# Performance work log

Measured on AMD Instinct MI355X. Metric: run time of the kernel, lower is better.

## Reference

```python
import jax, jax.numpy as jnp
import numpy as np

N, T, F = 20000, 8, 128
E = 320000
H_GCN, H_CONV, H_LSTM = 32, 64, 128


def setup_inputs() -> dict:
    key = jax.random.key(0)
    ks = jax.random.split(key, 16)
    s = lambda k, shape: jax.random.normal(k, shape, dtype=jnp.float32) * 0.05
    inp = {
        'x': jax.random.normal(ks[0], (N, T, F), dtype=jnp.float32),
        'edge_index': jax.random.randint(ks[1], (2, E), 0, N, dtype=jnp.int32),
        'gcn_W': s(ks[2], (F, H_GCN)),
        'gcn_b': s(ks[3], (H_GCN,)),
        'conv_W': s(ks[4], (H_CONV, H_GCN, 2)),
        'conv_b': s(ks[5], (H_CONV,)),
        'W_ih': s(ks[6], (4 * H_LSTM, H_CONV)),
        'W_hh': s(ks[7], (4 * H_LSTM, H_LSTM)),
        'b_ih': s(ks[8], (4 * H_LSTM,)),
        'b_hh': s(ks[9], (4 * H_LSTM,)),
        'fc1_W': s(ks[10], (64, H_LSTM)),
        'fc1_b': s(ks[11], (64,)),
        'fc2_W': s(ks[12], (F, 64)),
        'fc2_b': s(ks[13], (F,)),
    }
    return inp


def _forward(x, edge_index, gcn_W, gcn_b, conv_W, conv_b, W_ih, W_hh, b_ih, b_hh, fc1_W, fc1_b, fc2_W, fc2_b):
    n = x.shape[0]
    # ---- GCNConv (PyG semantics: linear, add self-loops, sym-normalized aggregate) ----
    loops = jnp.arange(n, dtype=edge_index.dtype)
    row = jnp.concatenate([edge_index[0], loops])  # source
    col = jnp.concatenate([edge_index[1], loops])  # target
    deg = jax.ops.segment_sum(jnp.ones_like(col, dtype=x.dtype), col, num_segments=n)
    dinv = jax.lax.rsqrt(deg)  # deg >= 1 thanks to self-loops
    norm = dinv[row] * dinv[col]  # [E+N]
    h = jnp.einsum('ntf,fo->nto', x, gcn_W)  # transform once for all timesteps
    msg = h[row] * norm[:, None, None]  # [E+N, T, 32]
    agg = jax.ops.segment_sum(msg, col, num_segments=n) + gcn_b
    g = jax.nn.relu(agg)  # [N, T, 32]; dropout is identity at inference
    # ---- Conv1d(32->64, k=2) over time ----
    xc = jnp.transpose(g, (0, 2, 1))  # [N, 32, T]
    y = jax.lax.conv_general_dilated(xc, conv_W, window_strides=(1,), padding='VALID',
                                     dimension_numbers=('NCH', 'OIH', 'NCH'))
    y = jax.nn.relu(y + conv_b[None, :, None])  # [N, 64, T-1]
    seq = jnp.transpose(y, (2, 0, 1))  # [T-1, N, 64]
    # ---- LSTM (torch gate order i, f, g, o) ----
    def step(carry, xt):
        hp, cp = carry
        z = xt @ W_ih.T + hp @ W_hh.T + (b_ih + b_hh)  # [N, 4H]
        i, f, gg, o = jnp.split(z, 4, axis=-1)
        c = jax.nn.sigmoid(f) * cp + jax.nn.sigmoid(i) * jnp.tanh(gg)
        hn = jax.nn.sigmoid(o) * jnp.tanh(c)
        return (hn, c), None
    h0 = jnp.zeros((n, H_LSTM), dtype=x.dtype)
    (hT, _), _ = jax.lax.scan(step, (h0, h0), seq)
    # ---- Head ----
    out = jax.nn.relu(hT @ fc1_W.T + fc1_b)
    out = jax.nn.sigmoid(out @ fc2_W.T + fc2_b)
    return out  # [N, num_features]


def reference(x, edge_index, gcn_W, gcn_b, conv_W, conv_b, W_ih, W_hh, b_ih, b_hh, fc1_W, fc1_b, fc2_W, fc2_b):
    return _forward(x, edge_index, gcn_W, gcn_b, conv_W, conv_b, W_ih, W_hh, b_ih, b_hh, fc1_W, fc1_b, fc2_W, fc2_b)
```

## Files before the change

### kernel.cpp

```cpp
#include <hip/hip_runtime.h>
#include <hip/hip_bf16.h>

#define T_STEPS 8
#define F_IN    128
#define H_GCN   32
#define H_CONV  64
#define H_LSTM  128

typedef __bf16 bf16x8 __attribute__((ext_vector_type(8)));
typedef float  f32x4  __attribute__((ext_vector_type(4)));
typedef unsigned short ushort8v __attribute__((ext_vector_type(8)));

#if __has_builtin(__builtin_amdgcn_exp2f)
__device__ __forceinline__ float exp2_f(float x) { return __builtin_amdgcn_exp2f(x); }
#else
__device__ __forceinline__ float exp2_f(float x) { return exp2f(x); }
#endif
#if __has_builtin(__builtin_amdgcn_rcpf)
__device__ __forceinline__ float rcp_f(float x) { return __builtin_amdgcn_rcpf(x); }
#else
__device__ __forceinline__ float rcp_f(float x) { return 1.f / x; }
#endif

#define NL2E  (-1.442695041f)
#define NL2E2 (-2.885390082f)

__device__ __forceinline__ float sigm_fast(float x) {
  return rcp_f(1.f + exp2_f(x * NL2E));
}

__device__ __forceinline__ float ubf(unsigned short u) {
  union { unsigned int i; float f; } v; v.i = ((unsigned int)u) << 16; return v.f;
}
__device__ __forceinline__ unsigned short bfb(float f) {
  __hip_bfloat16 b = __float2bfloat16(f);
  return __builtin_bit_cast(unsigned short, b);
}

__device__ __forceinline__ bf16x8 load_bf8(const __hip_bfloat16* p) {
  int4 v = *reinterpret_cast<const int4*>(p);
  return __builtin_bit_cast(bf16x8, v);
}

__global__ __launch_bounds__(256) void k_transform(const float* __restrict__ x,
                                                   const __hip_bfloat16* __restrict__ Wgt,
                                                   const float* __restrict__ dinv,
                                                   __hip_bfloat16* __restrict__ hs)
{
  int tid  = threadIdx.x;
  int wave = tid >> 6;
  int lane = tid & 63;
  int l15  = lane & 15;
  int lhi  = lane >> 4;
  long r0  = (long)blockIdx.x * 64 + wave * 16;

  bf16x8 bw[2][4];
  #pragma unroll
  for (int ct = 0; ct < 2; ++ct)
    #pragma unroll
    for (int ks = 0; ks < 4; ++ks)
      bw[ct][ks] = load_bf8(Wgt + (ct * 16 + l15) * 128 + ks * 32 + lhi * 8);

  const float* xp = x + (r0 + l15) * 128 + lhi * 8;
  f32x4 acc[2];
  acc[0] = (f32x4){0.f, 0.f, 0.f, 0.f};
  acc[1] = (f32x4){0.f, 0.f, 0.f, 0.f};

  #pragma unroll
  for (int ks = 0; ks < 4; ++ks) {
    float4 v0 = *reinterpret_cast<const float4*>(xp + ks * 32);
    float4 v1 = *reinterpret_cast<const float4*>(xp + ks * 32 + 4);
    bf16x8 a;
    a[0] = (__bf16)v0.x; a[1] = (__bf16)v0.y; a[2] = (__bf16)v0.z; a[3] = (__bf16)v0.w;
    a[4] = (__bf16)v1.x; a[5] = (__bf16)v1.y; a[6] = (__bf16)v1.z; a[7] = (__bf16)v1.w;
    acc[0] = __builtin_amdgcn_mfma_f32_16x16x32_bf16(a, bw[0][ks], acc[0], 0, 0, 0);
    acc[1] = __builtin_amdgcn_mfma_f32_16x16x32_bf16(a, bw[1][ks], acc[1], 0, 0, 0);
  }

  #pragma unroll
  for (int r = 0; r < 4; ++r) {
    long rr = r0 + lhi * 4 + r;
    float dv = dinv[rr >> 3];
    hs[rr * 32 + l15]      = __float2bfloat16(acc[0][r] * dv);
    hs[rr * 32 + 16 + l15] = __float2bfloat16(acc[1][r] * dv);
  }
}

__global__ void k_count_init(const int* __restrict__ col, int* __restrict__ cnt, int E,
                             int* __restrict__ adj, int N, int padE,
                             unsigned int* __restrict__ hz)
{
  int i = blockIdx.x * 256 + threadIdx.x;
  if (i < E) atomicAdd(&cnt[col[i]], 1);
  if (i < padE) adj[i] = N;
  int j = i - padE;
  if (j >= 0 && j < 128) hz[j] = 0u;
}

__global__ __launch_bounds__(1024) void k_scan(const int* __restrict__ cnt,
                                               int* __restrict__ row_ptr,
                                               int* __restrict__ cursor,
                                               float* __restrict__ dinv, int N)
{
  __shared__ int s[1024];
  int tid = threadIdx.x;
  const int CH = (N + 1023) >> 10;
  int i0 = tid * CH;
  int sum = 0;
  for (int j = 0; j < CH; ++j) {
    int i = i0 + j;
    if (i < N) sum += (cnt[i] + 15) & ~15;
  }
  s[tid] = sum;
  __syncthreads();
  #pragma unroll
  for (int off = 1; off < 1024; off <<= 1) {
    int t = (tid >= off) ? s[tid - off] : 0;
    __syncthreads();
    s[tid] += t;
    __syncthreads();
  }
  int run = (tid > 0) ? s[tid - 1] : 0;
  for (int j = 0; j < CH; ++j) {
    int i = i0 + j;
    if (i < N) {
      int v = cnt[i];
      cursor[i] = run;
      row_ptr[i] = run;
      dinv[i] = rsqrtf((float)v + 1.0f);
      run += (v + 15) & ~15;
      if (i == N - 1) row_ptr[N] = run;
    }
  }
}

__global__ void k_fill(const int* __restrict__ ei, int* __restrict__ cursor,
                       int* __restrict__ adj, int E)
{
  int e = blockIdx.x * 256 + threadIdx.x;
  if (e < E) {
    int r = ei[e], c = ei[E + e];
    int pos = atomicAdd(&cursor[c], 1);
    adj[pos] = r;
  }
}

__global__ __launch_bounds__(256) void k_gather(
    const int* __restrict__ row_ptr, const int* __restrict__ adj,
    const float* __restrict__ dinv, const __hip_bfloat16* __restrict__ hs,
    const float* __restrict__ gcnb,
    __hip_bfloat16* __restrict__ g, int N)
{
  int tid  = threadIdx.x;
  int wave = tid >> 6;
  int lane = tid & 63;

  int n = blockIdx.x * 4 + wave;
  int start = row_ptr[n], end = row_ptr[n + 1];
  float dn = dinv[n];

  const __hip_bfloat16* hl = hs + lane * 4;
  float acc0, acc1, acc2, acc3;
  {
    ushort4 hv = *reinterpret_cast<const ushort4*>(hl + (size_t)n * 256);
    acc0 = ubf(hv.x); acc1 = ubf(hv.y); acc2 = ubf(hv.z); acc3 = ubf(hv.w);
  }

  for (int base = start; base < end; base += 16) {
    int s0 = adj[base + 0],  s1 = adj[base + 1],  s2 = adj[base + 2],  s3 = adj[base + 3];
    int s4 = adj[base + 4],  s5 = adj[base + 5],  s6 = adj[base + 6],  s7 = adj[base + 7];
    int s8 = adj[base + 8],  s9 = adj[base + 9],  sa = adj[base + 10], sb = adj[base + 11];
    int sc = adj[base + 12], sd = adj[base + 13], se = adj[base + 14], sf = adj[base + 15];
    ushort4 r0 = *reinterpret_cast<const ushort4*>(hl + (size_t)s0 * 256);
    ushort4 r1 = *reinterpret_cast<const ushort4*>(hl + (size_t)s1 * 256);
    ushort4 r2 = *reinterpret_cast<const ushort4*>(hl + (size_t)s2 * 256);
    ushort4 r3 = *reinterpret_cast<const ushort4*>(hl + (size_t)s3 * 256);
    ushort4 r4 = *reinterpret_cast<const ushort4*>(hl + (size_t)s4 * 256);
    ushort4 r5 = *reinterpret_cast<const ushort4*>(hl + (size_t)s5 * 256);
    ushort4 r6 = *reinterpret_cast<const ushort4*>(hl + (size_t)s6 * 256);
    ushort4 r7 = *reinterpret_cast<const ushort4*>(hl + (size_t)s7 * 256);
    ushort4 r8 = *reinterpret_cast<const ushort4*>(hl + (size_t)s8 * 256);
    ushort4 r9 = *reinterpret_cast<const ushort4*>(hl + (size_t)s9 * 256);
    ushort4 ra = *reinterpret_cast<const ushort4*>(hl + (size_t)sa * 256);
    ushort4 rb = *reinterpret_cast<const ushort4*>(hl + (size_t)sb * 256);
    ushort4 rc = *reinterpret_cast<const ushort4*>(hl + (size_t)sc * 256);
    ushort4 rd = *reinterpret_cast<const ushort4*>(hl + (size_t)sd * 256);
    ushort4 re = *reinterpret_cast<const ushort4*>(hl + (size_t)se * 256);
    ushort4 rf = *reinterpret_cast<const ushort4*>(hl + (size_t)sf * 256);
    acc0 += ((ubf(r0.x) + ubf(r1.x)) + (ubf(r2.x) + ubf(r3.x))) + ((ubf(r4.x) + ubf(r5.x)) + (ubf(r6.x) + ubf(r7.x)))
          + ((ubf(r8.x) + ubf(r9.x)) + (ubf(ra.x) + ubf(rb.x))) + ((ubf(rc.x) + ubf(rd.x)) + (ubf(re.x) + ubf(rf.x)));
    acc1 += ((ubf(r0.y) + ubf(r1.y)) + (ubf(r2.y) + ubf(r3.y))) + ((ubf(r4.y) + ubf(r5.y)) + (ubf(r6.y) + ubf(r7.y)))
          + ((ubf(r8.y) + ubf(r9.y)) + (ubf(ra.y) + ubf(rb.y))) + ((ubf(rc.y) + ubf(rd.y)) + (ubf(re.y) + ubf(rf.y)));
    acc2 += ((ubf(r0.z) + ubf(r1.z)) + (ubf(r2.z) + ubf(r3.z))) + ((ubf(r4.z) + ubf(r5.z)) + (ubf(r6.z) + ubf(r7.z)))
          + ((ubf(r8.z) + ubf(r9.z)) + (ubf(ra.z) + ubf(rb.z))) + ((ubf(rc.z) + ubf(rd.z)) + (ubf(re.z) + ubf(rf.z)));
    acc3 += ((ubf(r0.w) + ubf(r1.w)) + (ubf(r2.w) + ubf(r3.w))) + ((ubf(r4.w) + ubf(r5.w)) + (ubf(r6.w) + ubf(r7.w)))
          + ((ubf(r8.w) + ubf(r9.w)) + (ubf(ra.w) + ubf(rb.w))) + ((ubf(rc.w) + ubf(rd.w)) + (ubf(re.w) + ubf(rf.w)));
  }

  int ci0 = (lane * 4) & 31;
  ushort4 o;
  o.x = bfb(fmaxf(fmaf(acc0, dn, gcnb[ci0 + 0]), 0.f));
  o.y = bfb(fmaxf(fmaf(acc1, dn, gcnb[ci0 + 1]), 0.f));
  o.z = bfb(fmaxf(fmaf(acc2, dn, gcnb[ci0 + 2]), 0.f));
  o.w = bfb(fmaxf(fmaf(acc3, dn, gcnb[ci0 + 3]), 0.f));
  *reinterpret_cast<ushort4*>(g + (size_t)n * 256 + lane * 4) = o;
}

__global__ __launch_bounds__(256) void k_conv(
    const __hip_bfloat16* __restrict__ g,
    const __hip_bfloat16* __restrict__ Wcb,
    const float* __restrict__ bc,
    __hip_bfloat16* __restrict__ seq, int N)
{
  __shared__ __hip_bfloat16 A[4][16][72];
  int tid  = threadIdx.x;
  int wave = tid >> 6;
  int lane = tid & 63;
  int l15  = lane & 15;
  int lhi  = lane >> 4;

  if (tid < 144) {
    int w = tid / 36, q = tid % 36;
    int row = 14 + q / 18, cc = (q % 18) * 4;
    *reinterpret_cast<uint2*>(&A[w][row][cc]) = make_uint2(0u, 0u);
  }

  {
    int f0 = tid * 8;
    ushort8v v = *reinterpret_cast<const ushort8v*>(g + (size_t)blockIdx.x * 2048 + f0);
    int n_local = f0 >> 8;
    int rem     = f0 & 255;
    int t_row   = rem >> 5;
    int ci0     = rem & 31;
    int w       = n_local >> 1;
    int rbase   = (n_local & 1) * 7;
    #pragma unroll
    for (int e = 0; e < 8; ++e) {
      unsigned short u = v[e];
      int k0 = (ci0 + e) * 2;
      if (t_row <= 6)
        *reinterpret_cast<unsigned short*>(&A[w][rbase + t_row][k0]) = u;
      if (t_row >= 1)
        *reinterpret_cast<unsigned short*>(&A[w][rbase + t_row - 1][k0 + 1]) = u;
    }
  }
  __syncthreads();

  bf16x8 bfr[2][4];
  #pragma unroll
  for (int ks = 0; ks < 2; ++ks)
    #pragma unroll
    for (int cg = 0; cg < 4; ++cg)
      bfr[ks][cg] = load_bf8(Wcb + (cg * 16 + l15) * 64 + ks * 32 + lhi * 8);

  f32x4 acc[4];
  #pragma unroll
  for (int cg = 0; cg < 4; ++cg) acc[cg] = (f32x4){0.f, 0.f, 0.f, 0.f};

  #pragma unroll
  for (int ks = 0; ks < 2; ++ks) {
    bf16x8 a = load_bf8(&A[wave][l15][ks * 32 + lhi * 8]);
    #pragma unroll
    for (int cg = 0; cg < 4; ++cg)
      acc[cg] = __builtin_amdgcn_mfma_f32_16x16x32_bf16(a, bfr[ks][cg], acc[cg], 0, 0, 0);
  }

  long n64 = (long)N * 64;
  #pragma unroll
  for (int r = 0; r < 4; ++r) {
    int rr = lhi * 4 + r;
    if (rr < 14) {
      int hi = rr >= 7 ? 1 : 0;
      int nl = wave * 2 + hi;
      int t  = rr - 7 * hi;
      long n = (long)blockIdx.x * 8 + nl;
      #pragma unroll
      for (int cg = 0; cg < 4; ++cg) {
        int co = cg * 16 + l15;
        seq[(long)t * n64 + n * 64 + co] = __float2bfloat16(fmaxf(acc[cg][r] + bc[co], 0.f));
      }
    }
  }
}

__global__ __launch_bounds__(256) void k_prep(const float* __restrict__ Wih, const float* __restrict__ Whh,
                       const float* __restrict__ bih, const float* __restrict__ bhh,
                       const float* __restrict__ fc1W, const float* __restrict__ fc2W,
                       const float* __restrict__ convW, const float* __restrict__ gcnW,
                       __hip_bfloat16* __restrict__ Wcat, float* __restrict__ bias,
                       __hip_bfloat16* __restrict__ W1b, __hip_bfloat16* __restrict__ W2b,
                       __hip_bfloat16* __restrict__ Wcb, __hip_bfloat16* __restrict__ Wgt)
{
  int i = blockIdx.x * 256 + threadIdx.x;
  if (i < 512 * 192) {
    int q = i / 192, k = i - q * 192;
    float v = (k < 64) ? Wih[q * 64 + k] : Whh[q * 128 + (k - 64)];
    Wcat[i] = __float2bfloat16(v);
  } else if (i < 512 * 192 + 64 * 128) {
    int j = i - 512 * 192;
    W1b[j] = __float2bfloat16(fc1W[j]);
  } else if (i < 512 * 192 + 64 * 128 + 128 * 64) {
    int j = i - 512 * 192 - 64 * 128;
    W2b[j] = __float2bfloat16(fc2W[j]);
  } else if (i < 512 * 192 + 64 * 128 + 128 * 64 + 64 * 64) {
    int j = i - 512 * 192 - 64 * 128 - 128 * 64;
    Wcb[j] = __float2bfloat16(convW[j]);
  } else if (i < 512 * 192 + 64 * 128 + 128 * 64 + 64 * 64 + 32 * 128) {
    int j = i - 512 * 192 - 64 * 128 - 128 * 64 - 64 * 64;
    int o = j >> 7, f = j & 127;
    Wgt[j] = __float2bfloat16(gcnW[f * 32 + o]);
  } else if (i < 512 * 192 + 64 * 128 + 128 * 64 + 64 * 64 + 32 * 128 + 512) {
    int j = i - 512 * 192 - 64 * 128 - 128 * 64 - 64 * 64 - 32 * 128;
    bias[j] = bih[j] + bhh[j];
  }
}

__global__ __launch_bounds__(512, 2) void k_lstm_head(
    const __hip_bfloat16* __restrict__ seq,
    const __hip_bfloat16* __restrict__ Wcat,
    const float* __restrict__ bias,
    const __hip_bfloat16* __restrict__ W1b,
    const float* __restrict__ fc1b,
    const __hip_bfloat16* __restrict__ W2b,
    const float* __restrict__ fc2b,
    float* __restrict__ out, int N)
{
  __shared__ __hip_bfloat16 h_lds[2][16][136];
  __shared__ __hip_bfloat16 s1_lds[16][72];
  int tid  = threadIdx.x;
  int wave = tid >> 6;
  int lane = tid & 63;
  int l15  = lane & 15;
  int lhi  = lane >> 4;
  long n0  = (long)blockIdx.x * 16;
  int hc   = wave * 16 + l15;

  bf16x8 bw[6][4];
  #pragma unroll
  for (int ks = 0; ks < 6; ++ks)
    #pragma unroll
    for (int gg = 0; gg < 4; ++gg)
      bw[ks][gg] = load_bf8(Wcat + (size_t)(gg * 128 + hc) * 192 + ks * 32 + lhi * 8);

  float kbi = bias[hc]       * NL2E;
  float kbf = bias[128 + hc] * NL2E;
  float kbg = bias[256 + hc] * NL2E2;
  float kbo = bias[384 + hc] * NL2E;
  float c[4] = {0.f, 0.f, 0.f, 0.f};

  const __hip_bfloat16* sp = seq + (n0 + l15) * 64 + lhi * 8;
  size_t tstr = (size_t)N * 64;
  bf16x8 ax0 = load_bf8(sp);
  bf16x8 ax1 = load_bf8(sp + 32);

  for (int t = 0; t < 7; ++t) {
    bf16x8 nx0, nx1;
    if (t < 6) {
      nx0 = load_bf8(sp + (size_t)(t + 1) * tstr);
      nx1 = load_bf8(sp + (size_t)(t + 1) * tstr + 32);
    }
    f32x4 acc[4];
    #pragma unroll
    for (int gg = 0; gg < 4; ++gg) acc[gg] = (f32x4){0.f, 0.f, 0.f, 0.f};

    #pragma unroll
    for (int gg = 0; gg < 4; ++gg)
      acc[gg] = __builtin_amdgcn_mfma_f32_16x16x32_bf16(ax0, bw[0][gg], acc[gg], 0, 0, 0);
    #pragma unroll
    for (int gg = 0; gg < 4; ++gg)
      acc[gg] = __builtin_amdgcn_mfma_f32_16x16x32_bf16(ax1, bw[1][gg], acc[gg], 0, 0, 0);

    if (t > 0) {
      const __hip_bfloat16* hb = &h_lds[(t + 1) & 1][0][0];
      #pragma unroll
      for (int ks = 2; ks < 6; ++ks) {
        bf16x8 a = load_bf8(hb + l15 * 136 + (ks - 2) * 32 + lhi * 8);
        #pragma unroll
        for (int gg = 0; gg < 4; ++gg)
          acc[gg] = __builtin_amdgcn_mfma_f32_16x16x32_bf16(a, bw[ks][gg], acc[gg], 0, 0, 0);
      }
    }

    __hip_bfloat16* hw = &h_lds[t & 1][0][0];
    #pragma unroll
    for (int r = 0; r < 4; ++r) {
      float si  = rcp_f(1.f + exp2_f(fmaf(acc[0][r], NL2E,  kbi)));
      float sf  = rcp_f(1.f + exp2_f(fmaf(acc[1][r], NL2E,  kbf)));
      float sg2 = rcp_f(1.f + exp2_f(fmaf(acc[2][r], NL2E2, kbg)));
      float so  = rcp_f(1.f + exp2_f(fmaf(acc[3][r], NL2E,  kbo)));
      float tg  = fmaf(2.f, sg2, -1.f);
      float cn  = fmaf(sf, c[r], si * tg);
      c[r] = cn;
      float sc2 = rcp_f(1.f + exp2_f(cn * NL2E2));
      float hn  = so * fmaf(2.f, sc2, -1.f);
      hw[(lhi * 4 + r) * 136 + hc] = __float2bfloat16(hn);
    }
    __syncthreads();

    ax0 = nx0; ax1 = nx1;
  }

  if (wave < 4) {
    int col1 = wave * 16 + l15;
    f32x4 acc1 = (f32x4){0.f, 0.f, 0.f, 0.f};
    #pragma unroll
    for (int ks = 0; ks < 4; ++ks) {
      int kb = ks * 32 + lhi * 8;
      bf16x8 a = load_bf8(&h_lds[0][l15][kb]);
      bf16x8 b = load_bf8(W1b + col1 * 128 + kb);
      acc1 = __builtin_amdgcn_mfma_f32_16x16x32_bf16(a, b, acc1, 0, 0, 0);
    }
    float b1 = fc1b[col1];
    #pragma unroll
    for (int r = 0; r < 4; ++r)
      s1_lds[lhi * 4 + r][col1] = __float2bfloat16(fmaxf(acc1[r] + b1, 0.f));
  }
  __syncthreads();

  {
    int c2 = wave * 16 + l15;
    f32x4 acc2 = (f32x4){0.f, 0.f, 0.f, 0.f};
    #pragma unroll
    for (int ks = 0; ks < 2; ++ks) {
      int kb = ks * 32 + lhi * 8;
      bf16x8 a = load_bf8(&s1_lds[l15][kb]);
      bf16x8 b = load_bf8(W2b + c2 * 64 + kb);
      acc2 = __builtin_amdgcn_mfma_f32_16x16x32_bf16(a, b, acc2, 0, 0, 0);
    }
    float b2 = fc2b[c2];
    #pragma unroll
    for (int r = 0; r < 4; ++r)
      out[(n0 + lhi * 4 + r) * 128 + c2] = sigm_fast(acc2[r] + b2);
  }
}

extern "C" void kernel_launch(void* const* d_in, const int* in_sizes, int n_in,
                              void* d_out, int out_size, void* d_ws, size_t ws_size,
                              hipStream_t stream)
{
  const float* x     = (const float*)d_in[0];
  const int*   ei    = (const int*)d_in[1];
  const float* gcnW  = (const float*)d_in[2];
  const float* gcnb  = (const float*)d_in[3];
  const float* convW = (const float*)d_in[4];
  const float* convb = (const float*)d_in[5];
  const float* Wih   = (const float*)d_in[6];
  const float* Whh   = (const float*)d_in[7];
  const float* bih   = (const float*)d_in[8];
  const float* bhh   = (const float*)d_in[9];
  const float* fc1W  = (const float*)d_in[10];
  const float* fc1b  = (const float*)d_in[11];
  const float* fc2W  = (const float*)d_in[12];
  const float* fc2b  = (const float*)d_in[13];

  const int N = in_sizes[0] / (T_STEPS * F_IN);
  const int E = in_sizes[1] / 2;
  const int padE = E + 16 * N;

  char* ws = (char*)d_ws;
  size_t off = 0;
  auto alloc = [&](size_t bytes) {
    void* p = ws + off;
    off = (off + bytes + 255) & ~(size_t)255;
    return p;
  };
  __hip_bfloat16* hs  = (__hip_bfloat16*)alloc((size_t)(N + 1) * 256 * 2);
  __hip_bfloat16* g   = (__hip_bfloat16*)alloc((size_t)N * 256 * 2);
  __hip_bfloat16* seq = (__hip_bfloat16*)alloc((size_t)7 * N * 64 * 2);
  int* cnt     = (int*)alloc((size_t)N * 4);
  int* row_ptr = (int*)alloc((size_t)(N + 1) * 4);
  int* cursor  = (int*)alloc((size_t)N * 4);
  float* dinv  = (float*)alloc((size_t)N * 4);
  int* adj     = (int*)alloc((size_t)padE * 4);
  __hip_bfloat16* Wcat = (__hip_bfloat16*)alloc(512 * 192 * 2);
  float* bias = (float*)alloc(512 * 4);
  __hip_bfloat16* W1b = (__hip_bfloat16*)alloc(64 * 128 * 2);
  __hip_bfloat16* W2b = (__hip_bfloat16*)alloc(128 * 64 * 2);
  __hip_bfloat16* Wcb = (__hip_bfloat16*)alloc(64 * 64 * 2);
  __hip_bfloat16* Wgt = (__hip_bfloat16*)alloc(32 * 128 * 2);

  hipMemsetAsync(cnt, 0, (size_t)N * 4, stream);

  const int PREP_TOT = 512 * 192 + 64 * 128 + 128 * 64 + 64 * 64 + 32 * 128 + 512;
  k_prep<<<(PREP_TOT + 255) / 256, 256, 0, stream>>>(Wih, Whh, bih, bhh, fc1W, fc2W, convW, gcnW,
                                                     Wcat, bias, W1b, W2b, Wcb, Wgt);
  k_count_init<<<(padE + 128 + 255) / 256, 256, 0, stream>>>(
      ei + E, cnt, E, adj, N, padE, (unsigned int*)(hs + (size_t)N * 256));
  k_scan<<<1, 1024, 0, stream>>>(cnt, row_ptr, cursor, dinv, N);
  k_transform<<<(N * T_STEPS) / 64, 256, 0, stream>>>(x, Wgt, dinv, hs);
  k_fill<<<(E + 255) / 256, 256, 0, stream>>>(ei, cursor, adj, E);
  k_gather<<<N / 4, 256, 0, stream>>>(row_ptr, adj, dinv, hs, gcnb, g, N);
  k_conv<<<N / 8, 256, 0, stream>>>(g, Wcb, convb, seq, N);
  k_lstm_head<<<N / 16, 512, 0, stream>>>(seq, Wcat, bias, W1b, fc1b, W2b, fc2b, (float*)d_out, N);
}
```

Before: 221.8 us.

## Process 32 nodes per LSTM block to reuse register-resident weights

The LSTM+head kernel now handles two 16-row node tiles per block instead of one, sharing the register-held W_ih/W_hh fragments across both tiles and halving the block count. This amortizes each block's load of the weight fragments and gives the MFMA units two independent accumulator chains to interleave. The head is reshaped so all 8 waves participate. In exchange, register pressure rises (double accumulators and cell state) under launch_bounds(512,2), which risks spills or lower occupancy. N/32 blocks also assumes N divides by 32.

Measured after the change: 216.4 us. -2.4%, faster.

```diff
diff --git a/kernel.cpp b/kernel.cpp
--- a/kernel.cpp
+++ b/kernel.cpp
@@ -325,14 +325,14 @@
     const float* __restrict__ fc2b,
     float* __restrict__ out, int N)
 {
-  __shared__ __hip_bfloat16 h_lds[2][16][136];
-  __shared__ __hip_bfloat16 s1_lds[16][72];
+  __shared__ __hip_bfloat16 h_lds[2][32][136];
+  __shared__ __hip_bfloat16 s1_lds[32][72];
   int tid  = threadIdx.x;
   int wave = tid >> 6;
   int lane = tid & 63;
   int l15  = lane & 15;
   int lhi  = lane >> 4;
-  long n0  = (long)blockIdx.x * 16;
+  long n0  = (long)blockIdx.x * 32;
   int hc   = wave * 16 + l15;
 
   bf16x8 bw[6][4];
@@ -346,91 +346,121 @@
   float kbf = bias[128 + hc] * NL2E;
   float kbg = bias[256 + hc] * NL2E2;
   float kbo = bias[384 + hc] * NL2E;
-  float c[4] = {0.f, 0.f, 0.f, 0.f};
-
-  const __hip_bfloat16* sp = seq + (n0 + l15) * 64 + lhi * 8;
+  float c0[4] = {0.f, 0.f, 0.f, 0.f};
+  float c1[4] = {0.f, 0.f, 0.f, 0.f};
+
+  const __hip_bfloat16* sp0 = seq + (n0 +      l15) * 64 + lhi * 8;
+  const __hip_bfloat16* sp1 = seq + (n0 + 16 + l15) * 64 + lhi * 8;
   size_t tstr = (size_t)N * 64;
-  bf16x8 ax0 = load_bf8(sp);
-  bf16x8 ax1 = load_bf8(sp + 32);
+  bf16x8 ax00 = load_bf8(sp0), ax01 = load_bf8(sp0 + 32);
+  bf16x8 ax10 = load_bf8(sp1), ax11 = load_bf8(sp1 + 32);
 
   for (int t = 0; t < 7; ++t) {
-    bf16x8 nx0, nx1;
+    bf16x8 nx00, nx01, nx10, nx11;
     if (t < 6) {
-      nx0 = load_bf8(sp + (size_t)(t + 1) * tstr);
-      nx1 = load_bf8(sp + (size_t)(t + 1) * tstr + 32);
-    }
-    f32x4 acc[4];
-    #pragma unroll
-    for (int gg = 0; gg < 4; ++gg) acc[gg] = (f32x4){0.f, 0.f, 0.f, 0.f};
-
-    #pragma unroll
-    for (int gg = 0; gg < 4; ++gg)
-      acc[gg] = __builtin_amdgcn_mfma_f32_16x16x32_bf16(ax0, bw[0][gg], acc[gg], 0, 0, 0);
-    #pragma unroll
-    for (int gg = 0; gg < 4; ++gg)
-      acc[gg] = __builtin_amdgcn_mfma_f32_16x16x32_bf16(ax1, bw[1][gg], acc[gg], 0, 0, 0);
+      nx00 = load_bf8(sp0 + (size_t)(t + 1) * tstr);
+      nx01 = load_bf8(sp0 + (size_t)(t + 1) * tstr + 32);
+      nx10 = load_bf8(sp1 + (size_t)(t + 1) * tstr);
+      nx11 = load_bf8(sp1 + (size_t)(t + 1) * tstr + 32);
+    }
+    f32x4 acc0[4], acc1[4];
+    #pragma unroll
+    for (int gg = 0; gg < 4; ++gg) {
+      acc0[gg] = (f32x4){0.f, 0.f, 0.f, 0.f};
+      acc1[gg] = (f32x4){0.f, 0.f, 0.f, 0.f};
+    }
+
+    #pragma unroll
+    for (int gg = 0; gg < 4; ++gg) {
+      acc0[gg] = __builtin_amdgcn_mfma_f32_16x16x32_bf16(ax00, bw[0][gg], acc0[gg], 0, 0, 0);
+      acc1[gg] = __builtin_amdgcn_mfma_f32_16x16x32_bf16(ax10, bw[0][gg], acc1[gg], 0, 0, 0);
+    }
+    #pragma unroll
+    for (int gg = 0; gg < 4; ++gg) {
+      acc0[gg] = __builtin_amdgcn_mfma_f32_16x16x32_bf16(ax01, bw[1][gg], acc0[gg], 0, 0, 0);
+      acc1[gg] = __builtin_amdgcn_mfma_f32_16x16x32_bf16(ax11, bw[1][gg], acc1[gg], 0, 0, 0);
+    }
 
     if (t > 0) {
       const __hip_bfloat16* hb = &h_lds[(t + 1) & 1][0][0];
       #pragma unroll
       for (int ks = 2; ks < 6; ++ks) {
-        bf16x8 a = load_bf8(hb + l15 * 136 + (ks - 2) * 32 + lhi * 8);
+        bf16x8 a0 = load_bf8(hb + (     l15) * 136 + (ks - 2) * 32 + lhi * 8);
+        bf16x8 a1 = load_bf8(hb + (16 + l15) * 136 + (ks - 2) * 32 + lhi * 8);
         #pragma unroll
-        for (int gg = 0; gg < 4; ++gg)
-          acc[gg] = __builtin_amdgcn_mfma_f32_16x16x32_bf16(a, bw[ks][gg], acc[gg], 0, 0, 0);
+        for (int gg = 0; gg < 4; ++gg) {
+          acc0[gg] = __builtin_amdgcn_mfma_f32_16x16x32_bf16(a0, bw[ks][gg], acc0[gg], 0, 0, 0);
+          acc1[gg] = __builtin_amdgcn_mfma_f32_16x16x32_bf16(a1, bw[ks][gg], acc1[gg], 0, 0, 0);
+        }
       }
     }
 
     __hip_bfloat16* hw = &h_lds[t & 1][0][0];
     #pragma unroll
     for (int r = 0; r < 4; ++r) {
-      float si  = rcp_f(1.f + exp2_f(fmaf(acc[0][r], NL2E,  kbi)));
-      float sf  = rcp_f(1.f + exp2_f(fmaf(acc[1][r], NL2E,  kbf)));
-      float sg2 = rcp_f(1.f + exp2_f(fmaf(acc[2][r], NL2E2, kbg)));
-      float so  = rcp_f(1.f + exp2_f(fmaf(acc[3][r], NL2E,  kbo)));
+      float si  = rcp_f(1.f + exp2_f(fmaf(acc0[0][r], NL2E,  kbi)));
+      float sf  = rcp_f(1.f + exp2_f(fmaf(acc0[1][r], NL2E,  kbf)));
+      float sg2 = rcp_f(1.f + exp2_f(fmaf(acc0[2][r], NL2E2, kbg)));
+      float so  = rcp_f(1.f + exp2_f(fmaf(acc0[3][r], NL2E,  kbo)));
       float tg  = fmaf(2.f, sg2, -1.f);
-      float cn  = fmaf(sf, c[r], si * tg);
-      c[r] = cn;
+      float cn  = fmaf(sf, c0[r], si * tg);
+      c0[r] = cn;
       float sc2 = rcp_f(1.f + exp2_f(cn * NL2E2));
-      float hn  = so * fmaf(2.f, sc2, -1.f);
-      hw[(lhi * 4 + r) * 136 + hc] = __float2bfloat16(hn);
+      hw[(lhi * 4 + r) * 136 + hc] = __float2bfloat16(so * fmaf(2.f, sc2, -1.f));
+    }
+    #pragma unroll
+    for (int r = 0; r < 4; ++r) {
+      float si  = rcp_f(1.f + exp2_f(fmaf(acc1[0][r], NL2E,  kbi)));
+      float sf  = rcp_f(1.f + exp2_f(fmaf(acc1[1][r], NL2E,  kbf)));
+      float sg2 = rcp_f(1.f + exp2_f(fmaf(acc1[2][r], NL2E2, kbg)));
+      float so  = rcp_f(1.f + exp2_f(fmaf(acc1[3][r], NL2E,  kbo)));
+      float tg  = fmaf(2.f, sg2, -1.f);
+      float cn  = fmaf(sf, c1[r], si * tg);
+      c1[r] = cn;
+      float sc2 = rcp_f(1.f + exp2_f(cn * NL2E2));
+      hw[(16 + lhi * 4 + r) * 136 + hc] = __float2bfloat16(so * fmaf(2.f, sc2, -1.f));
     }
     __syncthreads();
 
-    ax0 = nx0; ax1 = nx1;
-  }
-
-  if (wave < 4) {
-    int col1 = wave * 16 + l15;
-    f32x4 acc1 = (f32x4){0.f, 0.f, 0.f, 0.f};
+    ax00 = nx00; ax01 = nx01; ax10 = nx10; ax11 = nx11;
+  }
+
+  {
+    int m1   = wave >> 2;
+    int col1 = (wave & 3) * 16 + l15;
+    f32x4 acc1v = (f32x4){0.f, 0.f, 0.f, 0.f};
     #pragma unroll
     for (int ks = 0; ks < 4; ++ks) {
       int kb = ks * 32 + lhi * 8;
-      bf16x8 a = load_bf8(&h_lds[0][l15][kb]);
+      bf16x8 a = load_bf8(&h_lds[0][m1 * 16 + l15][kb]);
       bf16x8 b = load_bf8(W1b + col1 * 128 + kb);
-      acc1 = __builtin_amdgcn_mfma_f32_16x16x32_bf16(a, b, acc1, 0, 0, 0);
+      acc1v = __builtin_amdgcn_mfma_f32_16x16x32_bf16(a, b, acc1v, 0, 0, 0);
     }
     float b1 = fc1b[col1];
     #pragma unroll
     for (int r = 0; r < 4; ++r)
-      s1_lds[lhi * 4 + r][col1] = __float2bfloat16(fmaxf(acc1[r] + b1, 0.f));
+      s1_lds[m1 * 16 + lhi * 4 + r][col1] = __float2bfloat16(fmaxf(acc1v[r] + b1, 0.f));
   }
   __syncthreads();
 
   {
-    int c2 = wave * 16 + l15;
-    f32x4 acc2 = (f32x4){0.f, 0.f, 0.f, 0.f};
-    #pragma unroll
-    for (int ks = 0; ks < 2; ++ks) {
-      int kb = ks * 32 + lhi * 8;
-      bf16x8 a = load_bf8(&s1_lds[l15][kb]);
-      bf16x8 b = load_bf8(W2b + c2 * 64 + kb);
-      acc2 = __builtin_amdgcn_mfma_f32_16x16x32_bf16(a, b, acc2, 0, 0, 0);
-    }
-    float b2 = fc2b[c2];
-    #pragma unroll
-    for (int r = 0; r < 4; ++r)
-      out[(n0 + lhi * 4 + r) * 128 + c2] = sigm_fast(acc2[r] + b2);
+    int m2 = wave >> 2;
+    #pragma unroll
+    for (int half = 0; half < 2; ++half) {
+      int c2 = (wave & 3) * 16 + half * 64 + l15;
+      f32x4 acc2 = (f32x4){0.f, 0.f, 0.f, 0.f};
+      #pragma unroll
+      for (int ks = 0; ks < 2; ++ks) {
+        int kb = ks * 32 + lhi * 8;
+        bf16x8 a = load_bf8(&s1_lds[m2 * 16 + l15][kb]);
+        bf16x8 b = load_bf8(W2b + c2 * 64 + kb);
+        acc2 = __builtin_amdgcn_mfma_f32_16x16x32_bf16(a, b, acc2, 0, 0, 0);
+      }
+      float b2 = fc2b[c2];
+      #pragma unroll
+      for (int r = 0; r < 4; ++r)
+        out[(n0 + m2 * 16 + lhi * 4 + r) * 128 + c2] = sigm_fast(acc2[r] + b2);
+    }
   }
 }
 
@@ -491,5 +521,5 @@
   k_fill<<<(E + 255) / 256, 256, 0, stream>>>(ei, cursor, adj, E);
   k_gather<<<N / 4, 256, 0, stream>>>(row_ptr, adj, dinv, hs, gcnb, g, N);
   k_conv<<<N / 8, 256, 0, stream>>>(g, Wcb, convb, seq, N);
-  k_lstm_head<<<N / 16, 512, 0, stream>>>(seq, Wcat, bias, W1b, fc1b, W2b, fc2b, (float*)d_out, N);
-}
+  k_lstm_head<<<N / 32, 512, 0, stream>>>(seq, Wcat, bias, W1b, fc1b, W2b, fc2b, (float*)d_out, N);
+}
```

## Process 80 nodes per LSTM block to amortize register-resident weights

Applied to the files above, without the earlier changes.

The LSTM+head kernel now handles five 16-node tiles per block instead of one, reusing the register-held Wcat fragments across all five tiles and cutting the grid from N/16 to N/80 blocks (250 blocks). This amortizes the per-block weight loads and gives each wave more independent MFMA work per barrier. In exchange, accumulator and cell-state register usage grows by about 5x, which may cause spills under launch_bounds(512,2). The small grid may also leave many of the GPU's CUs idle. The next-timestep input prefetch was dropped as well.

Result: faster. 205.2 us (-7.5%).

```diff
diff --git a/kernel.cpp b/kernel.cpp
--- a/kernel.cpp
+++ b/kernel.cpp
@@ -325,14 +325,14 @@
     const float* __restrict__ fc2b,
     float* __restrict__ out, int N)
 {
-  __shared__ __hip_bfloat16 h_lds[2][16][136];
-  __shared__ __hip_bfloat16 s1_lds[16][72];
+  __shared__ __hip_bfloat16 h_lds[2][80][136];
+  __shared__ __hip_bfloat16 s1_lds[80][72];
   int tid  = threadIdx.x;
   int wave = tid >> 6;
   int lane = tid & 63;
   int l15  = lane & 15;
   int lhi  = lane >> 4;
-  long n0  = (long)blockIdx.x * 16;
+  long n0  = (long)blockIdx.x * 80;
   int hc   = wave * 16 + l15;
 
   bf16x8 bw[6][4];
@@ -346,91 +346,106 @@
   float kbf = bias[128 + hc] * NL2E;
   float kbg = bias[256 + hc] * NL2E2;
   float kbo = bias[384 + hc] * NL2E;
-  float c[4] = {0.f, 0.f, 0.f, 0.f};
-
-  const __hip_bfloat16* sp = seq + (n0 + l15) * 64 + lhi * 8;
+  float c[5][4];
+  #pragma unroll
+  for (int g = 0; g < 5; ++g)
+    #pragma unroll
+    for (int r = 0; r < 4; ++r) c[g][r] = 0.f;
+
   size_t tstr = (size_t)N * 64;
-  bf16x8 ax0 = load_bf8(sp);
-  bf16x8 ax1 = load_bf8(sp + 32);
+  const __hip_bfloat16* spb = seq + (n0 + l15) * 64 + lhi * 8;
 
   for (int t = 0; t < 7; ++t) {
-    bf16x8 nx0, nx1;
-    if (t < 6) {
-      nx0 = load_bf8(sp + (size_t)(t + 1) * tstr);
-      nx1 = load_bf8(sp + (size_t)(t + 1) * tstr + 32);
-    }
-    f32x4 acc[4];
-    #pragma unroll
-    for (int gg = 0; gg < 4; ++gg) acc[gg] = (f32x4){0.f, 0.f, 0.f, 0.f};
-
-    #pragma unroll
-    for (int gg = 0; gg < 4; ++gg)
-      acc[gg] = __builtin_amdgcn_mfma_f32_16x16x32_bf16(ax0, bw[0][gg], acc[gg], 0, 0, 0);
-    #pragma unroll
-    for (int gg = 0; gg < 4; ++gg)
-      acc[gg] = __builtin_amdgcn_mfma_f32_16x16x32_bf16(ax1, bw[1][gg], acc[gg], 0, 0, 0);
+    f32x4 acc[5][4];
+    #pragma unroll
+    for (int g = 0; g < 5; ++g)
+      #pragma unroll
+      for (int gg = 0; gg < 4; ++gg)
+        acc[g][gg] = (f32x4){0.f, 0.f, 0.f, 0.f};
+
+    #pragma unroll
+    for (int g = 0; g < 5; ++g) {
+      const __hip_bfloat16* sp = spb + (size_t)t * tstr + (size_t)g * 16 * 64;
+      bf16x8 a0 = load_bf8(sp);
+      bf16x8 a1 = load_bf8(sp + 32);
+      #pragma unroll
+      for (int gg = 0; gg < 4; ++gg)
+        acc[g][gg] = __builtin_amdgcn_mfma_f32_16x16x32_bf16(a0, bw[0][gg], acc[g][gg], 0, 0, 0);
+      #pragma unroll
+      for (int gg = 0; gg < 4; ++gg)
+        acc[g][gg] = __builtin_amdgcn_mfma_f32_16x16x32_bf16(a1, bw[1][gg], acc[g][gg], 0, 0, 0);
+    }
 
     if (t > 0) {
       const __hip_bfloat16* hb = &h_lds[(t + 1) & 1][0][0];
       #pragma unroll
       for (int ks = 2; ks < 6; ++ks) {
-        bf16x8 a = load_bf8(hb + l15 * 136 + (ks - 2) * 32 + lhi * 8);
         #pragma unroll
-        for (int gg = 0; gg < 4; ++gg)
-          acc[gg] = __builtin_amdgcn_mfma_f32_16x16x32_bf16(a, bw[ks][gg], acc[gg], 0, 0, 0);
+        for (int g = 0; g < 5; ++g) {
+          bf16x8 a = load_bf8(hb + (g * 16 + l15) * 136 + (ks - 2) * 32 + lhi * 8);
+          #pragma unroll
+          for (int gg = 0; gg < 4; ++gg)
+            acc[g][gg] = __builtin_amdgcn_mfma_f32_16x16x32_bf16(a, bw[ks][gg], acc[g][gg], 0, 0, 0);
+        }
       }
     }
 
     __hip_bfloat16* hw = &h_lds[t & 1][0][0];
     #pragma unroll
-    for (int r = 0; r < 4; ++r) {
-      float si  = rcp_f(1.f + exp2_f(fmaf(acc[0][r], NL2E,  kbi)));
-      float sf  = rcp_f(1.f + exp2_f(fmaf(acc[1][r], NL2E,  kbf)));
-      float sg2 = rcp_f(1.f + exp2_f(fmaf(acc[2][r], NL2E2, kbg)));
-      float so  = rcp_f(1.f + exp2_f(fmaf(acc[3][r], NL2E,  kbo)));
-      float tg  = fmaf(2.f, sg2, -1.f);
-      float cn  = fmaf(sf, c[r], si * tg);
-      c[r] = cn;
-      float sc2 = rcp_f(1.f + exp2_f(cn * NL2E2));
-      float hn  = so * fmaf(2.f, sc2, -1.f);
-      hw[(lhi * 4 + r) * 136 + hc] = __float2bfloat16(hn);
+    for (int g = 0; g < 5; ++g) {
+      #pragma unroll
+      for (int r = 0; r < 4; ++r) {
+        float si  = rcp_f(1.f + exp2_f(fmaf(acc[g][0][r], NL2E,  kbi)));
+        float sf  = rcp_f(1.f + exp2_f(fmaf(acc[g][1][r], NL2E,  kbf)));
+        float sg2 = rcp_f(1.f + exp2_f(fmaf(acc[g][2][r], NL2E2, kbg)));
+        float so  = rcp_f(1.f + exp2_f(fmaf(acc[g][3][r], NL2E,  kbo)));
+        float tg  = fmaf(2.f, sg2, -1.f);
+        float cn  = fmaf(sf, c[g][r], si * tg);
+        c[g][r] = cn;
+        float sc2 = rcp_f(1.f + exp2_f(cn * NL2E2));
+        hw[(g * 16 + lhi * 4 + r) * 136 + hc] = __float2bfloat16(so * fmaf(2.f, sc2, -1.f));
+      }
     }
     __syncthreads();
-
-    ax0 = nx0; ax1 = nx1;
   }
 
   if (wave < 4) {
     int col1 = wave * 16 + l15;
-    f32x4 acc1 = (f32x4){0.f, 0.f, 0.f, 0.f};
-    #pragma unroll
-    for (int ks = 0; ks < 4; ++ks) {
-      int kb = ks * 32 + lhi * 8;
-      bf16x8 a = load_bf8(&h_lds[0][l15][kb]);
-      bf16x8 b = load_bf8(W1b + col1 * 128 + kb);
-      acc1 = __builtin_amdgcn_mfma_f32_16x16x32_bf16(a, b, acc1, 0, 0, 0);
-    }
     float b1 = fc1b[col1];
     #pragma unroll
-    for (int r = 0; r < 4; ++r)
-      s1_lds[lhi * 4 + r][col1] = __float2bfloat16(fmaxf(acc1[r] + b1, 0.f));
+    for (int g = 0; g < 5; ++g) {
+      f32x4 acc1v = (f32x4){0.f, 0.f, 0.f, 0.f};
+      #pragma unroll
+      for (int ks = 0; ks < 4; ++ks) {
+        int kb = ks * 32 + lhi * 8;
+        bf16x8 a = load_bf8(&h_lds[0][g * 16 + l15][kb]);
+        bf16x8 b = load_bf8(W1b + col1 * 128 + kb);
+        acc1v = __builtin_amdgcn_mfma_f32_16x16x32_bf16(a, b, acc1v, 0, 0, 0);
+      }
+      #pragma unroll
+      for (int r = 0; r < 4; ++r)
+        s1_lds[g * 16 + lhi * 4 + r][col1] = __float2bfloat16(fmaxf(acc1v[r] + b1, 0.f));
+    }
   }
   __syncthreads();
 
   {
     int c2 = wave * 16 + l15;
-    f32x4 acc2 = (f32x4){0.f, 0.f, 0.f, 0.f};
-    #pragma unroll
-    for (int ks = 0; ks < 2; ++ks) {
-      int kb = ks * 32 + lhi * 8;
-      bf16x8 a = load_bf8(&s1_lds[l15][kb]);
-      bf16x8 b = load_bf8(W2b + c2 * 64 + kb);
-      acc2 = __builtin_amdgcn_mfma_f32_16x16x32_bf16(a, b, acc2, 0, 0, 0);
-    }
     float b2 = fc2b[c2];
     #pragma unroll
-    for (int r = 0; r < 4; ++r)
-      out[(n0 + lhi * 4 + r) * 128 + c2] = sigm_fast(acc2[r] + b2);
+    for (int g = 0; g < 5; ++g) {
+      f32x4 acc2 = (f32x4){0.f, 0.f, 0.f, 0.f};
+      #pragma unroll
+      for (int ks = 0; ks < 2; ++ks) {
+        int kb = ks * 32 + lhi * 8;
+        bf16x8 a = load_bf8(&s1_lds[g * 16 + l15][kb]);
+        bf16x8 b = load_bf8(W2b + c2 * 64 + kb);
+        acc2 = __builtin_amdgcn_mfma_f32_16x16x32_bf16(a, b, acc2, 0, 0, 0);
+      }
+      #pragma unroll
+      for (int r = 0; r < 4; ++r)
+        out[(n0 + g * 16 + lhi * 4 + r) * 128 + c2] = sigm_fast(acc2[r] + b2);
+    }
   }
 }
 
@@ -491,5 +506,5 @@
   k_fill<<<(E + 255) / 256, 256, 0, stream>>>(ei, cursor, adj, E);
   k_gather<<<N / 4, 256, 0, stream>>>(row_ptr, adj, dinv, hs, gcnb, g, N);
   k_conv<<<N / 8, 256, 0, stream>>>(g, Wcb, convb, seq, N);
-  k_lstm_head<<<N / 16, 512, 0, stream>>>(seq, Wcat, bias, W1b, fc1b, W2b, fc2b, (float*)d_out, N);
-}
+  k_lstm_head<<<N / 80, 512, 0, stream>>>(seq, Wcat, bias, W1b, fc1b, W2b, fc2b, (float*)d_out, N);
+}
```
